# Kernel optimization log

Measured on AMD Instinct MI355X. Metric: run time of the kernel, lower is better.

## Reference

```python
import jax, jax.numpy as jnp
import numpy as np

B, T, F, H = 4, 2048, 512, 8
DK = F // H


def setup_inputs() -> dict:
    key = jax.random.key(0)
    ks = jax.random.split(key, 12)
    s = 1.0 / np.sqrt(F)
    return {
        "query": jax.random.normal(ks[0], (B, T, F), jnp.float32),
        "key": jax.random.normal(ks[1], (B, T, F), jnp.float32),
        "value": jax.random.normal(ks[2], (B, T, F), jnp.float32),
        "attn_mask": jax.random.randint(ks[3], (B, 1, T), 0, 2, jnp.int32),
        "Wq": jax.random.uniform(ks[4], (F, F), jnp.float32, -s, s),
        "bq": jax.random.uniform(ks[5], (F,), jnp.float32, -s, s),
        "Wk": jax.random.uniform(ks[6], (F, F), jnp.float32, -s, s),
        "bk": jax.random.uniform(ks[7], (F,), jnp.float32, -s, s),
        "Wv": jax.random.uniform(ks[8], (F, F), jnp.float32, -s, s),
        "bv": jax.random.uniform(ks[9], (F,), jnp.float32, -s, s),
        "Wo": jax.random.uniform(ks[10], (F, F), jnp.float32, -s, s),
        "bo": jax.random.uniform(ks[11], (F,), jnp.float32, -s, s),
    }


def reference(query, key, value, attn_mask, Wq, bq, Wk, bk, Wv, bv, Wo, bo):
    b = query.shape[0]
    # QKV projections -> (b, h, t, d_k)
    q = (query @ Wq.T + bq).reshape(b, -1, H, DK).transpose(0, 2, 1, 3)
    k = (key @ Wk.T + bk).reshape(b, -1, H, DK).transpose(0, 2, 1, 3)
    v = (value @ Wv.T + bv).reshape(b, -1, H, DK).transpose(0, 2, 1, 3)
    scores = jnp.einsum("bhqd,bhkd->bhqk", q, k) / np.sqrt(DK)
    # mask (b,1,t2) -> (b,1,1,t2); masked where mask == 0
    m = (attn_mask[:, None, :, :] == 0)
    min_val = jnp.finfo(scores.dtype).min
    scores = jnp.where(m, min_val, scores)
    attn = jnp.where(m, 0.0, jax.nn.softmax(scores, axis=-1))
    # dropout is identity in eval mode
    x = jnp.einsum("bhqk,bhkd->bhqd", attn, v)
    x = x.transpose(0, 2, 1, 3).reshape(b, -1, H * DK)
    return x @ Wo.T + bo
```

## Files before the change

### kernel.cpp

```cpp
#include <hip/hip_runtime.h>
#include <hip/hip_bf16.h>
#include <stdint.h>

#define B_ 4
#define T_ 2048
#define F_ 512
#define H_ 8
#define DK_ 64
#define BT_ (B_*T_)

typedef short bf16x8 __attribute__((ext_vector_type(8)));
typedef short s16x4 __attribute__((ext_vector_type(4)));
typedef float f32x4 __attribute__((ext_vector_type(4)));
typedef float f32x16 __attribute__((ext_vector_type(16)));

__device__ __forceinline__ unsigned short f2bf(float f) {
  union { float f; unsigned u; } v; v.f = f;
  return (unsigned short)((v.u + 0x7fffu + ((v.u >> 16) & 1u)) >> 16);
}

__device__ __forceinline__ unsigned cvtpk(float lo, float hi) {
  unsigned w;
  asm("v_cvt_pk_bf16_f32 %0, %1, %2" : "=v"(w) : "v"(lo), "v"(hi));
  return w;
}

__device__ __forceinline__ void gload_lds16(const void* g, void* l) {
  __builtin_amdgcn_global_load_lds((const __attribute__((address_space(1))) void*)g,
                                   (__attribute__((address_space(3))) void*)l, 16, 0, 0);
}

__global__ void convert_scan(const float* __restrict__ wq, const float* __restrict__ wk,
                             const float* __restrict__ wv, const float* __restrict__ wo,
                             const int* __restrict__ mask,
                             unsigned short* __restrict__ dst, int* __restrict__ invidx,
                             int* __restrict__ nbuf) {
  const int seg = blockIdx.y;
  const int tid = threadIdx.x;
  if (seg == 4) {
    if (blockIdx.x >= 4) return;
    const int b = blockIdx.x;
    __shared__ int cnt[256];
    const int base = b * T_ + tid * 8;
    int4 a = *(const int4*)(mask + base);
    int4 d = *(const int4*)(mask + base + 4);
    int m[8] = {a.x, a.y, a.z, a.w, d.x, d.y, d.z, d.w};
    int c = 0;
#pragma unroll
    for (int i = 0; i < 8; ++i) c += (m[i] != 0);
    cnt[tid] = c;
    __syncthreads();
    for (int off = 1; off < 256; off <<= 1) {
      int v = (tid >= off) ? cnt[tid - off] : 0;
      __syncthreads();
      cnt[tid] += v;
      __syncthreads();
    }
    int excl = cnt[tid] - c;
#pragma unroll
    for (int i = 0; i < 8; ++i)
      if (m[i]) { invidx[b * T_ + excl] = tid * 8 + i; ++excl; }
    if (tid == 255) nbuf[b] = cnt[255];
    return;
  }
  const float* src = seg == 0 ? wq : (seg == 1 ? wk : (seg == 2 ? wv : wo));
  unsigned short* out = dst + (size_t)seg * F_ * F_;
  const int idx = (blockIdx.x * 256 + tid) * 8;
  float4 a = *(const float4*)(src + idx);
  float4 b = *(const float4*)(src + idx + 4);
  union { unsigned w[4]; bf16x8 v; } t;
  t.w[0] = cvtpk(a.x, a.y); t.w[1] = cvtpk(a.z, a.w);
  t.w[2] = cvtpk(b.x, b.y); t.w[3] = cvtpk(b.z, b.w);
  *(bf16x8*)(out + idx) = t.v;
}

__global__ __launch_bounds__(256, 3) void gemm_qkv(
    const float* __restrict__ qin, const float* __restrict__ kin, const float* __restrict__ vin,
    const unsigned short* __restrict__ Wbase,
    const float* __restrict__ bq, const float* __restrict__ bk, const float* __restrict__ bv,
    const int* __restrict__ invidx, const int* __restrict__ nbuf,
    unsigned short* __restrict__ projq, unsigned short* __restrict__ kc,
    unsigned short* __restrict__ vt, float qscale) {
  const int id0 = blockIdx.x;
  const int id = (id0 & 7) * 96 + (id0 >> 3);
  const int p = id >> 8, l = id & 255;
  const int tid = threadIdx.x;
  const int wid = tid >> 6, lane = tid & 63;
  const int lr = lane & 15, lg = lane >> 4;
  const int wr = wid >> 1, wc = wid & 1;
  const int n0 = (l & 3) * 128;

  const float* Af;
  const float* bias;
  float sc = 1.0f;
  int obase, j0 = 0, b = 0, nb = T_;
  if (p == 0) {
    obase = (l >> 2) * 128;
    Af = qin; bias = bq; sc = qscale;
  } else {
    b = l >> 6;
    j0 = ((l >> 2) & 15) * 128;
    nb = nbuf[b];
    if (j0 >= ((nb + 63) & ~63)) return;
    obase = b * T_ + j0;
    Af = (p == 1) ? kin : vin;
    bias = (p == 1) ? bk : bv;
  }
  const unsigned short* W = Wbase + (size_t)p * F_ * F_;

  __shared__ __align__(16) unsigned short As[128 * 64];
  __shared__ __align__(16) unsigned short Bs[128 * 64];

  int srcrow[4];
#pragma unroll
  for (int i = 0; i < 4; ++i) {
    const int r = (i * 256 + tid) >> 3;
    if (p == 0) srcrow[i] = obase + r;
    else {
      int j = j0 + r;
      if (j >= nb) j = nb - 1;
      srcrow[i] = b * T_ + invidx[b * T_ + j];
    }
  }

  float4 aR[4][2];
  auto loadA = [&](int k0) {
#pragma unroll
    for (int i = 0; i < 4; ++i) {
      const int s = (i * 256 + tid) & 7;
      const float* sp = Af + (size_t)srcrow[i] * F_ + k0 + s * 8;
      aR[i][0] = *(const float4*)sp;
      aR[i][1] = *(const float4*)(sp + 4);
    }
  };
  auto writeA = [&]() {
#pragma unroll
    for (int i = 0; i < 4; ++i) {
      const int ch = i * 256 + tid;
      const int r = ch >> 3, s = ch & 7;
      union { unsigned w[4]; bf16x8 v; } t;
      t.w[0] = cvtpk(aR[i][0].x, aR[i][0].y); t.w[1] = cvtpk(aR[i][0].z, aR[i][0].w);
      t.w[2] = cvtpk(aR[i][1].x, aR[i][1].y); t.w[3] = cvtpk(aR[i][1].z, aR[i][1].w);
      *(bf16x8*)&As[r * 64 + ((s ^ (r & 7)) * 8)] = t.v;
    }
  };
  auto stageB = [&](int k0) {
#pragma unroll
    for (int i = 0; i < 4; ++i) {
      const int ch = i * 256 + tid;
      const int r = ch >> 3, s = ch & 7;
      gload_lds16(W + (size_t)(n0 + r) * F_ + k0 + ((s ^ (r & 7)) * 8),
                  &Bs[(i * 256 + wid * 64) * 8]);
    }
  };

  f32x4 acc[4][4] = {};
  loadA(0);
  for (int k0 = 0; k0 < F_; k0 += 64) {
    stageB(k0);
    writeA();
    __syncthreads();
    if (k0 + 64 < F_) loadA(k0 + 64);

#pragma unroll
    for (int kk = 0; kk < 2; ++kk) {
      bf16x8 af[4], bf[4];
      const int slotA = (kk * 4 + lg) ^ (lr & 7);
#pragma unroll
      for (int m = 0; m < 4; ++m)
        af[m] = *(const bf16x8*)&As[(wr * 64 + m * 16 + lr) * 64 + slotA * 8];
#pragma unroll
      for (int n = 0; n < 4; ++n)
        bf[n] = *(const bf16x8*)&Bs[(wc * 64 + n * 16 + lr) * 64 + slotA * 8];
#pragma unroll
      for (int m = 0; m < 4; ++m)
#pragma unroll
        for (int n = 0; n < 4; ++n)
          acc[m][n] = __builtin_amdgcn_mfma_f32_16x16x32_bf16(af[m], bf[n], acc[m][n], 0, 0, 0);
    }
    __syncthreads();
  }

  if (p == 2) {
#pragma unroll
    for (int n = 0; n < 4; ++n) {
      const int col = n0 + wc * 64 + n * 16 + lr;
      const float bvv = bias[col];
      unsigned short* vrow = vt + ((size_t)(b * 8 + (col >> 6)) * 64 + (col & 63)) * T_;
#pragma unroll
      for (int m = 0; m < 4; ++m) {
        const int kv = j0 + wr * 64 + m * 16 + lg * 4;
        union { unsigned short u[4]; s16x4 v; } ov;
#pragma unroll
        for (int j = 0; j < 4; ++j) ov.u[j] = f2bf(acc[m][n][j] + bvv);
        *(s16x4*)(vrow + kv) = ov.v;
      }
    }
  } else {
    unsigned short* outp = (p == 0) ? projq : kc;
#pragma unroll
    for (int n = 0; n < 4; ++n) {
      const int col = n0 + wc * 64 + n * 16 + lr;
      const float bvv = bias[col];
#pragma unroll
      for (int m = 0; m < 4; ++m) {
        const int rbase = obase + wr * 64 + m * 16 + lg * 4;
#pragma unroll
        for (int j = 0; j < 4; ++j)
          outp[(size_t)(rbase + j) * F_ + col] = f2bf((acc[m][n][j] + bvv) * sc);
      }
    }
  }
}

__global__ __launch_bounds__(256, 3) void gemm_out(
    const unsigned short* __restrict__ Abf, const unsigned short* __restrict__ W,
    const float* __restrict__ bias, float* __restrict__ outf) {
  const int id0 = blockIdx.x;
  const int l = (id0 & 7) * 64 + (id0 >> 3);
  const int m0 = (l >> 2) * 64, n0 = (l & 3) * 128;
  const int tid = threadIdx.x;
  const int wid = tid >> 6, lane = tid & 63;
  const int lr = lane & 15, lg = lane >> 4;
  const int wr = wid >> 1, wc = wid & 1;

  __shared__ __align__(16) unsigned short As[64 * 64];
  __shared__ __align__(16) unsigned short Bs[128 * 64];

  auto stage = [&](int k0) {
#pragma unroll
    for (int i = 0; i < 2; ++i) {
      const int ch = i * 256 + tid;
      const int r = ch >> 3, s = ch & 7;
      gload_lds16(Abf + (size_t)(m0 + r) * F_ + k0 + ((s ^ (r & 7)) * 8),
                  &As[(i * 256 + wid * 64) * 8]);
    }
#pragma unroll
    for (int i = 0; i < 4; ++i) {
      const int ch = i * 256 + tid;
      const int r = ch >> 3, s = ch & 7;
      gload_lds16(W + (size_t)(n0 + r) * F_ + k0 + ((s ^ (r & 7)) * 8),
                  &Bs[(i * 256 + wid * 64) * 8]);
    }
  };

  f32x4 acc[2][4] = {};
  for (int k0 = 0; k0 < F_; k0 += 64) {
    stage(k0);
    __syncthreads();
#pragma unroll
    for (int kk = 0; kk < 2; ++kk) {
      bf16x8 af[2], bf[4];
      const int slotA = (kk * 4 + lg) ^ (lr & 7);
#pragma unroll
      for (int m = 0; m < 2; ++m)
        af[m] = *(const bf16x8*)&As[(wr * 32 + m * 16 + lr) * 64 + slotA * 8];
#pragma unroll
      for (int n = 0; n < 4; ++n)
        bf[n] = *(const bf16x8*)&Bs[(wc * 64 + n * 16 + lr) * 64 + slotA * 8];
#pragma unroll
      for (int m = 0; m < 2; ++m)
#pragma unroll
        for (int n = 0; n < 4; ++n)
          acc[m][n] = __builtin_amdgcn_mfma_f32_16x16x32_bf16(af[m], bf[n], acc[m][n], 0, 0, 0);
    }
    __syncthreads();
  }

#pragma unroll
  for (int n = 0; n < 4; ++n) {
    const int col = n0 + wc * 64 + n * 16 + lr;
    const float bvv = bias[col];
#pragma unroll
    for (int m = 0; m < 2; ++m) {
      const int rbase = m0 + wr * 32 + m * 16 + lg * 4;
#pragma unroll
      for (int j = 0; j < 4; ++j)
        outf[(size_t)(rbase + j) * F_ + col] = acc[m][n][j] + bvv;
    }
  }
}

__global__ __launch_bounds__(512, 1) void attn_kernel(
    const unsigned short* __restrict__ Qp,
    const unsigned short* __restrict__ Kp,
    const unsigned short* __restrict__ Vt,
    const int* __restrict__ nbuf,
    unsigned short* __restrict__ X) {
  const int tid = threadIdx.x, wid = tid >> 6, lane = tid & 63;
  const int la = lane & 31, hi = lane >> 5;
  const int id = blockIdx.x;
  const int swz = (id & 7) * 32 + (id >> 3);
  const int bh = swz >> 3, qb = swz & 7;
  const int b = bh >> 3, h = bh & 7;
  const int qrow = qb * 256 + wid * 32 + la;
  const int nb = nbuf[b];
  const int nt = (nb + 127) >> 7;

  __shared__ __align__(16) unsigned short Ks[3][128 * 64];
  __shared__ __align__(16) unsigned short Vs[3][64 * 128];

  bf16x8 qf[4];
#pragma unroll
  for (int kk = 0; kk < 4; ++kk)
    qf[kk] = *(const bf16x8*)(Qp + (size_t)(b * T_ + qrow) * F_ + h * DK_ + kk * 16 + hi * 8);

  union { unsigned short u[8]; bf16x8 v; } ones;
#pragma unroll
  for (int j = 0; j < 8; ++j) ones.u[j] = 0x3F80;

  f32x16 oacc[2] = {};
  f32x16 dacc = {};

  auto stage = [&](int buf, int kv0) {
#pragma unroll
    for (int i = 0; i < 2; ++i) {
      const int ch = i * 512 + tid;
      const int r = ch >> 3, s = ch & 7;
      gload_lds16(Kp + (size_t)(b * T_ + kv0 + r) * F_ + h * DK_ + ((s ^ (r & 7)) * 8),
                  &Ks[buf][(i * 512 + wid * 64) * 8]);
      const int d = ch >> 4, s2 = ch & 15;
      gload_lds16(Vt + ((size_t)bh * DK_ + d) * T_ + kv0 + ((s2 ^ (d & 15)) * 8),
                  &Vs[buf][(i * 512 + wid * 64) * 8]);
    }
  };

  if (nt > 0) {
    stage(0, 0);
    if (nt > 1) stage(1, 128);

    int cur = 0;
    for (int t = 0; t < nt; ++t) {
      if (t + 1 < nt) asm volatile("s_waitcnt vmcnt(4)" ::: "memory");
      else            asm volatile("s_waitcnt vmcnt(0)" ::: "memory");
      __builtin_amdgcn_s_barrier();
      __builtin_amdgcn_sched_barrier(0);
      if (t + 2 < nt) {
        int nxt = cur + 2; if (nxt >= 3) nxt -= 3;
        stage(nxt, (t + 2) * 128);
      }
      const int kv0 = t * 128;

      f32x16 sb[4];
      __builtin_amdgcn_s_setprio(1);
#pragma unroll
      for (int n = 0; n < 4; ++n) {
        bf16x8 kf[4];
#pragma unroll
        for (int kk = 0; kk < 4; ++kk)
          kf[kk] = *(const bf16x8*)&Ks[cur][(n * 32 + la) * 64 + ((((kk << 1) | hi) ^ (la & 7)) * 8)];
        f32x16 s = {};
#pragma unroll
        for (int kk = 0; kk < 4; ++kk)
          s = __builtin_amdgcn_mfma_f32_32x32x16_bf16(kf[kk], qf[kk], s, 0, 0, 0);
        sb[n] = s;
      }
      __builtin_amdgcn_s_setprio(0);

      if (kv0 + 128 > nb) {
        const int kvb = kv0 + 4 * hi;
#pragma unroll
        for (int n = 0; n < 4; ++n)
#pragma unroll
          for (int r = 0; r < 16; ++r) {
            const int kv = kvb + n * 32 + (r & 3) + 8 * (r >> 2);
            if (kv >= nb) sb[n][r] = -__builtin_inff();
          }
      }
#pragma unroll
      for (int n = 0; n < 4; ++n)
#pragma unroll
        for (int r = 0; r < 16; ++r)
          sb[n][r] = __builtin_amdgcn_exp2f(sb[n][r]);

      unsigned lowr[4][2][2], uppr[4][2][2];
#pragma unroll
      for (int n = 0; n < 4; ++n)
#pragma unroll
        for (int gg = 0; gg < 2; ++gg)
#pragma unroll
          for (int hh = 0; hh < 2; ++hh) {
            unsigned xE = cvtpk(sb[n][4 * (2 * gg) + 2 * hh], sb[n][4 * (2 * gg) + 2 * hh + 1]);
            unsigned xO = cvtpk(sb[n][4 * (2 * gg + 1) + 2 * hh], sb[n][4 * (2 * gg + 1) + 2 * hh + 1]);
            asm("v_permlane32_swap_b32 %0, %1" : "+v"(xE), "+v"(xO));
            lowr[n][gg][hh] = xE;
            uppr[n][gg][hh] = xO;
          }

#pragma unroll
      for (int kt = 0; kt < 8; ++kt) {
        const int n = kt >> 1, gg = kt & 1;
        union { unsigned w[4]; bf16x8 v; } pf;
        pf.w[0] = lowr[n][gg][0]; pf.w[1] = lowr[n][gg][1];
        pf.w[2] = uppr[n][gg][0]; pf.w[3] = uppr[n][gg][1];
        __builtin_amdgcn_s_setprio(1);
        dacc = __builtin_amdgcn_mfma_f32_32x32x16_bf16(ones.v, pf.v, dacc, 0, 0, 0);
#pragma unroll
        for (int m = 0; m < 2; ++m) {
          const int d = m * 32 + la;
          bf16x8 vfr = *(const bf16x8*)&Vs[cur][d * 128 + ((((kt << 1) | hi) ^ (d & 15)) * 8)];
          oacc[m] = __builtin_amdgcn_mfma_f32_32x32x16_bf16(vfr, pf.v, oacc[m], 0, 0, 0);
        }
        __builtin_amdgcn_s_setprio(0);
      }

      cur = (cur + 1 < 3) ? cur + 1 : 0;
    }
  }

  const float inv = 1.0f / fmaxf(dacc[0], 1e-37f);
#pragma unroll
  for (int m = 0; m < 2; ++m)
#pragma unroll
    for (int g = 0; g < 4; ++g) {
      union { unsigned short u[4]; s16x4 v; } ov;
#pragma unroll
      for (int j = 0; j < 4; ++j) ov.u[j] = f2bf(oacc[m][4 * g + j] * inv);
      *(s16x4*)(X + (size_t)(b * T_ + qrow) * F_ + h * DK_ + m * 32 + 8 * g + 4 * hi) = ov.v;
    }
}

extern "C" void kernel_launch(void* const* d_in, const int* in_sizes, int n_in,
                              void* d_out, int out_size, void* d_ws, size_t ws_size,
                              hipStream_t stream) {
  const float* q  = (const float*)d_in[0];
  const float* k  = (const float*)d_in[1];
  const float* v  = (const float*)d_in[2];
  const int* mask = (const int*)d_in[3];
  const float* Wq = (const float*)d_in[4];
  const float* bq = (const float*)d_in[5];
  const float* Wk = (const float*)d_in[6];
  const float* bk = (const float*)d_in[7];
  const float* Wv = (const float*)d_in[8];
  const float* bv = (const float*)d_in[9];
  const float* Wo = (const float*)d_in[10];
  const float* bo = (const float*)d_in[11];
  float* out = (float*)d_out;

  unsigned short* ws = (unsigned short*)d_ws;
  unsigned short* wts   = ws;
  unsigned short* projq = wts + (size_t)4 * F_ * F_;
  unsigned short* kc    = projq + (size_t)BT_ * F_;
  unsigned short* vt    = kc + (size_t)BT_ * F_;
  unsigned short* xbuf  = vt + (size_t)BT_ * F_;
  int* invidx  = (int*)(xbuf + (size_t)BT_ * F_);
  int* nbuf    = invidx + BT_;

  const float kQScale = 0.18033688011112042f;

  convert_scan<<<dim3(128, 5, 1), 256, 0, stream>>>(
      Wq, Wk, Wv, Wo, mask, wts, invidx, nbuf);
  gemm_qkv<<<dim3(768, 1, 1), 256, 0, stream>>>(
      q, k, v, wts, bq, bk, bv, invidx, nbuf, projq, kc, vt, kQScale);
  attn_kernel<<<dim3(256, 1, 1), 512, 0, stream>>>(
      projq, kc, vt, nbuf, xbuf);
  gemm_out<<<dim3(512, 1, 1), 256, 0, stream>>>(
      xbuf, wts + (size_t)3 * F_ * F_, bo, out);
}
```

Baseline: 68.68 us.

## Process two query groups per wave in attention to reuse K/V LDS fragments

Halves the attention block to 256 threads and gives each wave 64 query rows (two 32-row groups) instead of 32. Each wave loads K fragments from LDS once and reuses them for both query groups, and shares each V fragment across both groups' PV MFMAs. The staging loop and waitcnt are adjusted for the smaller thread count. This cuts LDS read traffic per MFMA but greatly increases register pressure and reduces the number of waves available to hide latency.

```diff
diff --git a/kernel.cpp b/kernel.cpp
--- a/kernel.cpp
+++ b/kernel.cpp
@@ -281,7 +281,7 @@
   }
 }
 
-__global__ __launch_bounds__(512, 1) void attn_kernel(
+__global__ __launch_bounds__(256, 1) void attn_kernel(
     const unsigned short* __restrict__ Qp,
     const unsigned short* __restrict__ Kp,
     const unsigned short* __restrict__ Vt,
@@ -293,35 +293,42 @@
   const int swz = (id & 7) * 32 + (id >> 3);
   const int bh = swz >> 3, qb = swz & 7;
   const int b = bh >> 3, h = bh & 7;
-  const int qrow = qb * 256 + wid * 32 + la;
+  const int qbase = qb * 256 + wid * 64;
   const int nb = nbuf[b];
   const int nt = (nb + 127) >> 7;
 
   __shared__ __align__(16) unsigned short Ks[3][128 * 64];
   __shared__ __align__(16) unsigned short Vs[3][64 * 128];
 
-  bf16x8 qf[4];
-#pragma unroll
-  for (int kk = 0; kk < 4; ++kk)
-    qf[kk] = *(const bf16x8*)(Qp + (size_t)(b * T_ + qrow) * F_ + h * DK_ + kk * 16 + hi * 8);
+  bf16x8 qf[2][4];
+#pragma unroll
+  for (int gq = 0; gq < 2; ++gq)
+#pragma unroll
+    for (int kk = 0; kk < 4; ++kk)
+      qf[gq][kk] = *(const bf16x8*)(Qp + (size_t)(b * T_ + qbase + gq * 32 + la) * F_ +
+                                    h * DK_ + kk * 16 + hi * 8);
 
   union { unsigned short u[8]; bf16x8 v; } ones;
 #pragma unroll
   for (int j = 0; j < 8; ++j) ones.u[j] = 0x3F80;
 
-  f32x16 oacc[2] = {};
-  f32x16 dacc = {};
+  f32x16 oacc[2][2] = {};
+  f32x16 dacc[2] = {};
 
   auto stage = [&](int buf, int kv0) {
 #pragma unroll
-    for (int i = 0; i < 2; ++i) {
-      const int ch = i * 512 + tid;
+    for (int i = 0; i < 4; ++i) {
+      const int ch = i * 256 + tid;
       const int r = ch >> 3, s = ch & 7;
       gload_lds16(Kp + (size_t)(b * T_ + kv0 + r) * F_ + h * DK_ + ((s ^ (r & 7)) * 8),
-                  &Ks[buf][(i * 512 + wid * 64) * 8]);
+                  &Ks[buf][(i * 256 + wid * 64) * 8]);
+    }
+#pragma unroll
+    for (int i = 0; i < 4; ++i) {
+      const int ch = i * 256 + tid;
       const int d = ch >> 4, s2 = ch & 15;
       gload_lds16(Vt + ((size_t)bh * DK_ + d) * T_ + kv0 + ((s2 ^ (d & 15)) * 8),
-                  &Vs[buf][(i * 512 + wid * 64) * 8]);
+                  &Vs[buf][(i * 256 + wid * 64) * 8]);
     }
   };
 
@@ -331,7 +338,7 @@
 
     int cur = 0;
     for (int t = 0; t < nt; ++t) {
-      if (t + 1 < nt) asm volatile("s_waitcnt vmcnt(4)" ::: "memory");
+      if (t + 1 < nt) asm volatile("s_waitcnt vmcnt(8)" ::: "memory");
       else            asm volatile("s_waitcnt vmcnt(0)" ::: "memory");
       __builtin_amdgcn_s_barrier();
       __builtin_amdgcn_sched_barrier(0);
@@ -341,65 +348,80 @@
       }
       const int kv0 = t * 128;
 
-      f32x16 sb[4];
+      bf16x8 kf[4][4];
+#pragma unroll
+      for (int n = 0; n < 4; ++n)
+#pragma unroll
+        for (int kk = 0; kk < 4; ++kk)
+          kf[n][kk] = *(const bf16x8*)&Ks[cur][(n * 32 + la) * 64 + ((((kk << 1) | hi) ^ (la & 7)) * 8)];
+
+      f32x16 sb[2][4];
       __builtin_amdgcn_s_setprio(1);
 #pragma unroll
-      for (int n = 0; n < 4; ++n) {
-        bf16x8 kf[4];
-#pragma unroll
-        for (int kk = 0; kk < 4; ++kk)
-          kf[kk] = *(const bf16x8*)&Ks[cur][(n * 32 + la) * 64 + ((((kk << 1) | hi) ^ (la & 7)) * 8)];
-        f32x16 s = {};
-#pragma unroll
-        for (int kk = 0; kk < 4; ++kk)
-          s = __builtin_amdgcn_mfma_f32_32x32x16_bf16(kf[kk], qf[kk], s, 0, 0, 0);
-        sb[n] = s;
-      }
+      for (int gq = 0; gq < 2; ++gq)
+#pragma unroll
+        for (int n = 0; n < 4; ++n) {
+          f32x16 s = {};
+#pragma unroll
+          for (int kk = 0; kk < 4; ++kk)
+            s = __builtin_amdgcn_mfma_f32_32x32x16_bf16(kf[n][kk], qf[gq][kk], s, 0, 0, 0);
+          sb[gq][n] = s;
+        }
       __builtin_amdgcn_s_setprio(0);
 
       if (kv0 + 128 > nb) {
         const int kvb = kv0 + 4 * hi;
 #pragma unroll
+        for (int gq = 0; gq < 2; ++gq)
+#pragma unroll
+          for (int n = 0; n < 4; ++n)
+#pragma unroll
+            for (int r = 0; r < 16; ++r) {
+              const int kv = kvb + n * 32 + (r & 3) + 8 * (r >> 2);
+              if (kv >= nb) sb[gq][n][r] = -__builtin_inff();
+            }
+      }
+#pragma unroll
+      for (int gq = 0; gq < 2; ++gq)
+#pragma unroll
         for (int n = 0; n < 4; ++n)
 #pragma unroll
-          for (int r = 0; r < 16; ++r) {
-            const int kv = kvb + n * 32 + (r & 3) + 8 * (r >> 2);
-            if (kv >= nb) sb[n][r] = -__builtin_inff();
-          }
-      }
-#pragma unroll
-      for (int n = 0; n < 4; ++n)
-#pragma unroll
-        for (int r = 0; r < 16; ++r)
-          sb[n][r] = __builtin_amdgcn_exp2f(sb[n][r]);
-
-      unsigned lowr[4][2][2], uppr[4][2][2];
-#pragma unroll
-      for (int n = 0; n < 4; ++n)
-#pragma unroll
-        for (int gg = 0; gg < 2; ++gg)
-#pragma unroll
-          for (int hh = 0; hh < 2; ++hh) {
-            unsigned xE = cvtpk(sb[n][4 * (2 * gg) + 2 * hh], sb[n][4 * (2 * gg) + 2 * hh + 1]);
-            unsigned xO = cvtpk(sb[n][4 * (2 * gg + 1) + 2 * hh], sb[n][4 * (2 * gg + 1) + 2 * hh + 1]);
-            asm("v_permlane32_swap_b32 %0, %1" : "+v"(xE), "+v"(xO));
-            lowr[n][gg][hh] = xE;
-            uppr[n][gg][hh] = xO;
-          }
+          for (int r = 0; r < 16; ++r)
+            sb[gq][n][r] = __builtin_amdgcn_exp2f(sb[gq][n][r]);
+
+      unsigned lowr[2][4][2][2], uppr[2][4][2][2];
+#pragma unroll
+      for (int gq = 0; gq < 2; ++gq)
+#pragma unroll
+        for (int n = 0; n < 4; ++n)
+#pragma unroll
+          for (int gg = 0; gg < 2; ++gg)
+#pragma unroll
+            for (int hh = 0; hh < 2; ++hh) {
+              unsigned xE = cvtpk(sb[gq][n][4 * (2 * gg) + 2 * hh], sb[gq][n][4 * (2 * gg) + 2 * hh + 1]);
+              unsigned xO = cvtpk(sb[gq][n][4 * (2 * gg + 1) + 2 * hh], sb[gq][n][4 * (2 * gg + 1) + 2 * hh + 1]);
+              asm("v_permlane32_swap_b32 %0, %1" : "+v"(xE), "+v"(xO));
+              lowr[gq][n][gg][hh] = xE;
+              uppr[gq][n][gg][hh] = xO;
+            }
 
 #pragma unroll
       for (int kt = 0; kt < 8; ++kt) {
         const int n = kt >> 1, gg = kt & 1;
-        union { unsigned w[4]; bf16x8 v; } pf;
-        pf.w[0] = lowr[n][gg][0]; pf.w[1] = lowr[n][gg][1];
-        pf.w[2] = uppr[n][gg][0]; pf.w[3] = uppr[n][gg][1];
+        union { unsigned w[4]; bf16x8 v; } pf0, pf1;
+        pf0.w[0] = lowr[0][n][gg][0]; pf0.w[1] = lowr[0][n][gg][1];
+        pf0.w[2] = uppr[0][n][gg][0]; pf0.w[3] = uppr[0][n][gg][1];
+        pf1.w[0] = lowr[1][n][gg][0]; pf1.w[1] = lowr[1][n][gg][1];
+        pf1.w[2] = uppr[1][n][gg][0]; pf1.w[3] = uppr[1][n][gg][1];
         __builtin_amdgcn_s_setprio(1);
-        dacc = __builtin_amdgcn_mfma_f32_32x32x16_bf16(ones.v, pf.v, dacc, 0, 0, 0);
+        dacc[0] = __builtin_amdgcn_mfma_f32_32x32x16_bf16(ones.v, pf0.v, dacc[0], 0, 0, 0);
+        dacc[1] = __builtin_amdgcn_mfma_f32_32x32x16_bf16(ones.v, pf1.v, dacc[1], 0, 0, 0);
 #pragma unroll
         for (int m = 0; m < 2; ++m) {
           const int d = m * 32 + la;
           bf16x8 vfr = *(const bf16x8*)&Vs[cur][d * 128 + ((((kt << 1) | hi) ^ (d & 15)) * 8)];
-          oacc[m] = __builtin_amdgcn_mfma_f32_32x32x16_bf16(vfr, pf.v, oacc[m], 0, 0, 0);
+          oacc[0][m] = __builtin_amdgcn_mfma_f32_32x32x16_bf16(vfr, pf0.v, oacc[0][m], 0, 0, 0);
+          oacc[1][m] = __builtin_amdgcn_mfma_f32_32x32x16_bf16(vfr, pf1.v, oacc[1][m], 0, 0, 0);
         }
         __builtin_amdgcn_s_setprio(0);
       }
@@ -408,16 +430,20 @@
     }
   }
 
-  const float inv = 1.0f / fmaxf(dacc[0], 1e-37f);
-#pragma unroll
-  for (int m = 0; m < 2; ++m)
-#pragma unroll
-    for (int g = 0; g < 4; ++g) {
-      union { unsigned short u[4]; s16x4 v; } ov;
-#pragma unroll
-      for (int j = 0; j < 4; ++j) ov.u[j] = f2bf(oacc[m][4 * g + j] * inv);
-      *(s16x4*)(X + (size_t)(b * T_ + qrow) * F_ + h * DK_ + m * 32 + 8 * g + 4 * hi) = ov.v;
-    }
+#pragma unroll
+  for (int gq = 0; gq < 2; ++gq) {
+    const float inv = 1.0f / fmaxf(dacc[gq][0], 1e-37f);
+#pragma unroll
+    for (int m = 0; m < 2; ++m)
+#pragma unroll
+      for (int g = 0; g < 4; ++g) {
+        union { unsigned short u[4]; s16x4 v; } ov;
+#pragma unroll
+        for (int j = 0; j < 4; ++j) ov.u[j] = f2bf(oacc[gq][m][4 * g + j] * inv);
+        *(s16x4*)(X + (size_t)(b * T_ + qbase + gq * 32 + la) * F_ + h * DK_ +
+                  m * 32 + 8 * g + 4 * hi) = ov.v;
+      }
+  }
 }
 
 extern "C" void kernel_launch(void* const* d_in, const int* in_sizes, int n_in,
@@ -452,7 +478,7 @@
       Wq, Wk, Wv, Wo, mask, wts, invidx, nbuf);
   gemm_qkv<<<dim3(768, 1, 1), 256, 0, stream>>>(
       q, k, v, wts, bq, bk, bv, invidx, nbuf, projq, kc, vt, kQScale);
-  attn_kernel<<<dim3(256, 1, 1), 512, 0, stream>>>(
+  attn_kernel<<<dim3(256, 1, 1), 256, 0, stream>>>(
       projq, kc, vt, nbuf, xbuf);
   gemm_out<<<dim3(512, 1, 1), 256, 0, stream>>>(
       xbuf, wts + (size_t)3 * F_ * F_, bo, out);
```

Measured after the change: 80.24 us. +16.8%, slower.
